# Kernel tuning notes

Measured on AMD Instinct MI355X. Metric: run time of the kernel, lower is better.

Reference implementation:

```python
import jax, jax.numpy as jnp
import numpy as np

EPS = 1e-5


def _batchnorm(x, gamma, beta):
    # training-mode batch norm over the node axis, per feature channel
    mean = jnp.mean(x, axis=0)
    var = jnp.var(x, axis=0)  # biased variance, as torch uses for normalization
    return (x - mean) * jax.lax.rsqrt(var + EPS) * gamma + beta


def _gcn_conv(h, W, b, src, dst, norm, n_nodes):
    # h: [N, Fin] -> [N, Fout]; D^{-1/2}(A+I)D^{-1/2} (h W) + b
    h = h @ W                                   # [N, Fout]
    msgs = h[src] * norm[:, None]               # [E+N, Fout] gathered, normalized
    out = jax.ops.segment_sum(msgs, dst, num_segments=n_nodes)
    return out + b


def setup_inputs() -> dict:
    key = jax.random.key(0)
    ks = jax.random.split(key, 8)
    N, F, E, H = 50000, 512, 800000, 256
    inp = {
        "x": jax.random.normal(ks[0], (N, F), jnp.float32),
        "edge_index": jax.random.randint(ks[1], (2, E), 0, N, jnp.int64),
        "gamma1": jnp.ones((F,), jnp.float32),
        "beta1": jnp.zeros((F,), jnp.float32),
        "W1": jax.random.normal(ks[2], (F, H), jnp.float32) * (1.0 / np.sqrt(F)),
        "b1": jnp.zeros((H,), jnp.float32),
        "W2": jax.random.normal(ks[3], (H, H), jnp.float32) * (1.0 / np.sqrt(H)),
        "b2": jnp.zeros((H,), jnp.float32),
        "W3": jax.random.normal(ks[4], (H, H), jnp.float32) * (1.0 / np.sqrt(H)),
        "b3": jnp.zeros((H,), jnp.float32),
        "W4": jax.random.normal(ks[5], (H, H), jnp.float32) * (1.0 / np.sqrt(H)),
        "b4": jnp.zeros((H,), jnp.float32),
        "gamma2": jnp.ones((H,), jnp.float32),
        "beta2": jnp.zeros((H,), jnp.float32),
        "Wd": jax.random.normal(ks[6], (H, 5), jnp.float32) * (1.0 / np.sqrt(H)),
        "bd": jnp.zeros((5,), jnp.float32),
    }
    return inp


def reference(x, edge_index, gamma1, beta1, W1, b1, W2, b2, W3, b3, W4, b4,
              gamma2, beta2, Wd, bd):
    N = x.shape[0]
    loops = jnp.arange(N, dtype=edge_index.dtype)
    src = jnp.concatenate([edge_index[0], loops])
    dst = jnp.concatenate([edge_index[1], loops])
    deg = jax.ops.segment_sum(jnp.ones_like(src, dtype=x.dtype), dst, num_segments=N)
    dinv = jax.lax.rsqrt(deg)                    # deg >= 1 due to self-loops
    norm = dinv[src] * dinv[dst]                 # [E+N]

    h = _batchnorm(x, gamma1, beta1)
    h = _gcn_conv(h, W1, b1, src, dst, norm, N)
    h = _gcn_conv(h, W2, b2, src, dst, norm, N)
    h = _gcn_conv(h, W3, b3, src, dst, norm, N)
    h = _gcn_conv(h, W4, b4, src, dst, norm, N)
    h = _batchnorm(h, gamma2, beta2)
    # Flatten(start_dim=1) is identity on [N, 256]
    return jax.nn.sigmoid(h @ Wd + bd)           # [N, 5]
```

## Files before the change

### kernel.cpp

```cpp
#include <hip/hip_runtime.h>
#include <math.h>

#define BN_EPS 1e-5f

typedef float floatx4 __attribute__((ext_vector_type(4)));
typedef short shortx4 __attribute__((ext_vector_type(4)));
typedef short shortx8 __attribute__((ext_vector_type(8)));
typedef __bf16 bf16x8 __attribute__((ext_vector_type(8)));

__device__ __forceinline__ unsigned short f2b(float f) {
    unsigned int u = __builtin_bit_cast(unsigned int, f);
    u += 0x7fffu + ((u >> 16) & 1u);
    return (unsigned short)(u >> 16);
}
__device__ __forceinline__ float b2f(unsigned short s) {
    unsigned int u = ((unsigned int)s) << 16;
    return __builtin_bit_cast(float, u);
}
__device__ __forceinline__ float b2f_s(short s) { return b2f((unsigned short)s); }

__global__ __launch_bounds__(256)
void k_detect(const unsigned int* __restrict__ ei, int n_check, int* __restrict__ flag) {
    __shared__ int any;
    if (threadIdx.x == 0) any = 0;
    __syncthreads();
    for (int i = threadIdx.x; i < n_check; i += 256) {
        if (ei[2 * i + 1] != 0u) any = 1;
    }
    __syncthreads();
    if (threadIdx.x == 0) *flag = any;
}

__global__ __launch_bounds__(256)
void k_convert(const void* __restrict__ ei_raw, const int* __restrict__ flag,
               int* __restrict__ src, int* __restrict__ dst, int* __restrict__ cnt, int E) {
    int e = blockIdx.x * 256 + threadIdx.x;
    if (e >= E) return;
    int s, d;
    if (*flag) {
        const int* a = (const int*)ei_raw;
        s = a[e]; d = a[E + e];
    } else {
        const long long* a = (const long long*)ei_raw;
        s = (int)a[e]; d = (int)a[E + e];
    }
    src[e] = s;
    dst[e] = d;
    atomicAdd(&cnt[d], 1);
}

__global__ __launch_bounds__(1024)
void k_scan_sum(const int* __restrict__ cnt, int* __restrict__ bsum, int N) {
    __shared__ int s[1024];
    int i = blockIdx.x * 1024 + threadIdx.x;
    s[threadIdx.x] = (i < N) ? cnt[i] : 0;
    __syncthreads();
    for (int off = 512; off > 0; off >>= 1) {
        if (threadIdx.x < off) s[threadIdx.x] += s[threadIdx.x + off];
        __syncthreads();
    }
    if (threadIdx.x == 0) bsum[blockIdx.x] = s[0];
}

__global__ __launch_bounds__(1024)
void k_scan_part(int* __restrict__ bsum, int nb) {
    __shared__ int s[1024];
    int t = threadIdx.x;
    int v = (t < nb) ? bsum[t] : 0;
    s[t] = v;
    __syncthreads();
    for (int off = 1; off < 1024; off <<= 1) {
        int tmp = (t >= off) ? s[t - off] : 0;
        __syncthreads();
        s[t] += tmp;
        __syncthreads();
    }
    if (t < nb) bsum[t] = s[t] - v;
}

__global__ __launch_bounds__(1024)
void k_scan_final(const int* __restrict__ cnt, const int* __restrict__ bsum,
                  int* __restrict__ row_ptr, int* __restrict__ cursor,
                  float* __restrict__ dinv, int N) {
    __shared__ int s[1024];
    int b = blockIdx.x, t = threadIdx.x;
    int i = b * 1024 + t;
    int v = (i < N) ? cnt[i] : 0;
    s[t] = v;
    __syncthreads();
    for (int off = 1; off < 1024; off <<= 1) {
        int tmp = (t >= off) ? s[t - off] : 0;
        __syncthreads();
        s[t] += tmp;
        __syncthreads();
    }
    if (i < N) {
        int excl = bsum[b] + s[t] - v;
        row_ptr[i] = excl;
        cursor[i]  = excl;
        dinv[i] = rsqrtf((float)(v + 1));
        if (i == N - 1) row_ptr[N] = excl + v;
    }
}

__global__ __launch_bounds__(256)
void k_fill(const int* __restrict__ src, const int* __restrict__ dst,
            int* __restrict__ cursor, const float* __restrict__ dinv,
            int2* __restrict__ csr_sw, int E) {
    int e = blockIdx.x * 256 + threadIdx.x;
    if (e >= E) return;
    int s = src[e], d = dst[e];
    int p = atomicAdd(&cursor[d], 1);
    float w = dinv[s] * dinv[d];
    csr_sw[p] = make_int2(s, __builtin_bit_cast(int, w));
}

__global__ __launch_bounds__(256)
void k_bnstats_cast(const float* __restrict__ x, unsigned short* __restrict__ xb,
                    float* __restrict__ sum8, float* __restrict__ sumsq8,
                    int NQ, int F) {
    __shared__ float ls[512], lq[512];
    int t   = threadIdx.x;
    int tid = blockIdx.x * 256 + t;
    int G   = gridDim.x * 256;
    int cq  = tid & ((F >> 2) - 1);
    const floatx4* xv = (const floatx4*)x;
    shortx4* xo = (shortx4*)xb;

    float s0 = 0.f, s1 = 0.f, s2 = 0.f, s3 = 0.f;
    float q0 = 0.f, q1 = 0.f, q2 = 0.f, q3 = 0.f;

    int G4 = G << 2;
    int Qfull = NQ - (NQ % G4);
    int i = tid;
    for (; i < Qfull; i += G4) {
        floatx4 a = __builtin_nontemporal_load(&xv[i]);
        floatx4 b = __builtin_nontemporal_load(&xv[i + G]);
        floatx4 c = __builtin_nontemporal_load(&xv[i + 2 * G]);
        floatx4 d = __builtin_nontemporal_load(&xv[i + 3 * G]);
        shortx4 o;
        o[0] = (short)f2b(a[0]); o[1] = (short)f2b(a[1]);
        o[2] = (short)f2b(a[2]); o[3] = (short)f2b(a[3]);
        xo[i] = o;
        s0 += a[0]; s1 += a[1]; s2 += a[2]; s3 += a[3];
        q0 += a[0] * a[0]; q1 += a[1] * a[1]; q2 += a[2] * a[2]; q3 += a[3] * a[3];
        o[0] = (short)f2b(b[0]); o[1] = (short)f2b(b[1]);
        o[2] = (short)f2b(b[2]); o[3] = (short)f2b(b[3]);
        xo[i + G] = o;
        s0 += b[0]; s1 += b[1]; s2 += b[2]; s3 += b[3];
        q0 += b[0] * b[0]; q1 += b[1] * b[1]; q2 += b[2] * b[2]; q3 += b[3] * b[3];
        o[0] = (short)f2b(c[0]); o[1] = (short)f2b(c[1]);
        o[2] = (short)f2b(c[2]); o[3] = (short)f2b(c[3]);
        xo[i + 2 * G] = o;
        s0 += c[0]; s1 += c[1]; s2 += c[2]; s3 += c[3];
        q0 += c[0] * c[0]; q1 += c[1] * c[1]; q2 += c[2] * c[2]; q3 += c[3] * c[3];
        o[0] = (short)f2b(d[0]); o[1] = (short)f2b(d[1]);
        o[2] = (short)f2b(d[2]); o[3] = (short)f2b(d[3]);
        xo[i + 3 * G] = o;
        s0 += d[0]; s1 += d[1]; s2 += d[2]; s3 += d[3];
        q0 += d[0] * d[0]; q1 += d[1] * d[1]; q2 += d[2] * d[2]; q3 += d[3] * d[3];
    }
    for (; i < NQ; i += G) {
        floatx4 a = __builtin_nontemporal_load(&xv[i]);
        shortx4 o;
        o[0] = (short)f2b(a[0]); o[1] = (short)f2b(a[1]);
        o[2] = (short)f2b(a[2]); o[3] = (short)f2b(a[3]);
        xo[i] = o;
        s0 += a[0]; s1 += a[1]; s2 += a[2]; s3 += a[3];
        q0 += a[0] * a[0]; q1 += a[1] * a[1]; q2 += a[2] * a[2]; q3 += a[3] * a[3];
    }

    for (int c = t; c < F; c += 256) { ls[c] = 0.f; lq[c] = 0.f; }
    __syncthreads();
    atomicAdd(&ls[cq * 4 + 0], s0); atomicAdd(&ls[cq * 4 + 1], s1);
    atomicAdd(&ls[cq * 4 + 2], s2); atomicAdd(&ls[cq * 4 + 3], s3);
    atomicAdd(&lq[cq * 4 + 0], q0); atomicAdd(&lq[cq * 4 + 1], q1);
    atomicAdd(&lq[cq * 4 + 2], q2); atomicAdd(&lq[cq * 4 + 3], q3);
    __syncthreads();
    int rep = (blockIdx.x & 7) * F;
    for (int c = t; c < F; c += 256) {
        atomicAdd(&sum8[rep + c],   ls[c]);
        atomicAdd(&sumsq8[rep + c], lq[c]);
    }
}

__global__ __launch_bounds__(256)
void k_bnstats_b(const unsigned short* __restrict__ x, float* __restrict__ sum,
                 float* __restrict__ sumsq, int NG, int H) {
    __shared__ float ls[256], lq[256];
    int t   = threadIdx.x;
    int tid = blockIdx.x * 256 + t;
    int G   = gridDim.x * 256;
    int cg  = tid & ((H >> 3) - 1);
    const shortx8* xv = (const shortx8*)x;
    float s[8], q[8];
    #pragma unroll
    for (int j = 0; j < 8; ++j) { s[j] = 0.f; q[j] = 0.f; }

    int G2 = G << 1;
    int Qfull = NG - (NG % G2);
    int i = tid;
    for (; i < Qfull; i += G2) {
        shortx8 a = __builtin_nontemporal_load(&xv[i]);
        shortx8 b = __builtin_nontemporal_load(&xv[i + G]);
        #pragma unroll
        for (int j = 0; j < 8; ++j) {
            float fa = b2f_s(a[j]);
            float fb = b2f_s(b[j]);
            s[j] += fa + fb;
            q[j] += fa * fa + fb * fb;
        }
    }
    for (; i < NG; i += G) {
        shortx8 a = __builtin_nontemporal_load(&xv[i]);
        #pragma unroll
        for (int j = 0; j < 8; ++j) {
            float fa = b2f_s(a[j]);
            s[j] += fa; q[j] += fa * fa;
        }
    }

    ls[t] = 0.f; lq[t] = 0.f;
    __syncthreads();
    #pragma unroll
    for (int j = 0; j < 8; ++j) {
        atomicAdd(&ls[cg * 8 + j], s[j]);
        atomicAdd(&lq[cg * 8 + j], q[j]);
    }
    __syncthreads();
    int rep = (blockIdx.x & 3) * H;
    atomicAdd(&sum[rep + t],   ls[t]);
    atomicAdd(&sumsq[rep + t], lq[t]);
}

__global__ __launch_bounds__(256)
void k_bnfin(const float* __restrict__ sum, const float* __restrict__ sumsq,
             const float* __restrict__ gamma, const float* __restrict__ beta,
             float* __restrict__ a, float* __restrict__ b, int N, int F, int nrep) {
    int c = blockIdx.x * 256 + threadIdx.x;
    if (c >= F) return;
    float s = 0.f, ss = 0.f;
    for (int i = 0; i < nrep; ++i) { s += sum[i * F + c]; ss += sumsq[i * F + c]; }
    float m   = s / (float)N;
    float var = ss / (float)N - m * m;
    float rs  = rsqrtf(var + BN_EPS);
    float aa  = gamma[c] * rs;
    a[c] = aa;
    b[c] = beta[c] - m * aa;
}

__global__ __launch_bounds__(256)
void k_castWT4(const float* __restrict__ W1, const float* __restrict__ W2,
               const float* __restrict__ W3, const float* __restrict__ W4,
               unsigned short* __restrict__ T1, unsigned short* __restrict__ T2,
               unsigned short* __restrict__ T3, unsigned short* __restrict__ T4,
               const float* __restrict__ bna, int F, int H) {
    int i = blockIdx.x * 256 + threadIdx.x;
    int n1 = F * H, n2 = H * H;
    if (i < n1) {
        int n = i / F, k = i % F;
        T1[i] = f2b(W1[(size_t)k * H + n] * bna[k]);
        return;
    }
    const float* W; unsigned short* T; int j;
    if (i < n1 + n2)          { W = W2; T = T2; j = i - n1; }
    else if (i < n1 + 2 * n2) { W = W3; T = T3; j = i - n1 - n2; }
    else if (i < n1 + 3 * n2) { W = W4; T = T4; j = i - n1 - 2 * n2; }
    else return;
    int n = j / H, k = j % H;
    T[j] = f2b(W[(size_t)k * H + n]);
}

__global__ __launch_bounds__(256)
void k_cvec(const float* __restrict__ W1, const float* __restrict__ bnb,
            float* __restrict__ cvec, int F, int H) {
    int j = threadIdx.x;
    int kslice = F / 8;
    int k0 = blockIdx.x * kslice;
    float s = 0.f;
    for (int k = k0; k < k0 + kslice; ++k)
        s += bnb[k] * W1[(size_t)k * H + j];
    atomicAdd(&cvec[j], s);
}

__device__ __forceinline__ void glds16(const void* g, void* l) {
    __builtin_amdgcn_global_load_lds(
        (const __attribute__((address_space(1))) unsigned int*)g,
        (__attribute__((address_space(3))) unsigned int*)l, 16, 0, 0);
}

__global__ __launch_bounds__(256)
void k_gemm_bf16(const unsigned short* __restrict__ A, const unsigned short* __restrict__ Bt,
                 unsigned short* __restrict__ C, int K, int NC) {
    __shared__ unsigned short As[128 * 32];
    __shared__ unsigned short Bs[128 * 32];
    int tid  = threadIdx.x;
    int wave = tid >> 6, lane = tid & 63;
    int row0 = blockIdx.x * 128;
    int col0 = blockIdx.y * 128;
    int wr = (wave & 1) * 64;
    int wc = (wave >> 1) * 64;

    floatx4 acc[4][4];
    #pragma unroll
    for (int i = 0; i < 4; i++)
        #pragma unroll
        for (int j = 0; j < 4; j++) acc[i][j] = (floatx4){0.f, 0.f, 0.f, 0.f};

    int cA = tid * 16;
    int cB = cA + 4096;
    const char* Ab = (const char*)A;
    const char* Bb = (const char*)Bt;
    size_t a_off0 = (size_t)(row0 + (cA >> 6)) * K * 2 + (cA & 63);
    size_t a_off1 = (size_t)(row0 + (cB >> 6)) * K * 2 + (cB & 63);
    size_t b_off0 = (size_t)(col0 + (cA >> 6)) * K * 2 + (cA & 63);
    size_t b_off1 = (size_t)(col0 + (cB >> 6)) * K * 2 + (cB & 63);

    int lm  = lane & 15;
    int lk8 = (lane >> 4) * 8;

    for (int ks = 0; ks < K; ks += 32) {
        size_t koff = (size_t)ks * 2;
        glds16(Ab + a_off0 + koff, (char*)As + cA);
        glds16(Ab + a_off1 + koff, (char*)As + cA + 4096);
        glds16(Bb + b_off0 + koff, (char*)Bs + cA);
        glds16(Bb + b_off1 + koff, (char*)Bs + cA + 4096);
        __syncthreads();

        bf16x8 af[4], bfr[4];
        #pragma unroll
        for (int i = 0; i < 4; i++) {
            shortx8 s = *(const shortx8*)&As[(wr + i * 16 + lm) * 32 + lk8];
            af[i] = __builtin_bit_cast(bf16x8, s);
        }
        #pragma unroll
        for (int j = 0; j < 4; j++) {
            shortx8 s = *(const shortx8*)&Bs[(wc + j * 16 + lm) * 32 + lk8];
            bfr[j] = __builtin_bit_cast(bf16x8, s);
        }
        #pragma unroll
        for (int i = 0; i < 4; i++)
            #pragma unroll
            for (int j = 0; j < 4; j++)
                acc[i][j] = __builtin_amdgcn_mfma_f32_16x16x32_bf16(af[i], bfr[j], acc[i][j], 0, 0, 0);
        __syncthreads();
    }

    int crow = row0 + wr + (lane >> 4) * 4;
    int ccol = col0 + wc + lm;
    #pragma unroll
    for (int i = 0; i < 4; i++)
        #pragma unroll
        for (int j = 0; j < 4; j++)
            #pragma unroll
            for (int r = 0; r < 4; r++)
                C[(size_t)(crow + i * 16 + r) * NC + ccol + j * 16] = f2b(acc[i][j][r]);
}

__global__ __launch_bounds__(256)
void k_agg(const unsigned short* __restrict__ hin, unsigned short* __restrict__ hout,
           const int* __restrict__ row_ptr, const int2* __restrict__ csr_sw,
           const float* __restrict__ dinv, const float* __restrict__ bias,
           const float* __restrict__ cvec, int N) {
    const int H = 256;
    int node = blockIdx.x * 4 + (threadIdx.x >> 6);
    if (node >= N) return;
    int lane = threadIdx.x & 63;
    int half = lane >> 5;
    int f = (lane & 31) * 8;
    float acc[8];
    float ws;
    float di = dinv[node];
    if (half == 0) {
        shortx8 hv = *(const shortx8*)&hin[(size_t)node * H + f];
        float sl = di * di;
        ws = sl;
        #pragma unroll
        for (int j = 0; j < 8; ++j) acc[j] = b2f_s(hv[j]) * sl;
    } else {
        ws = 0.f;
        #pragma unroll
        for (int j = 0; j < 8; ++j) acc[j] = 0.f;
    }
    int e0 = row_ptr[node], e1 = row_ptr[node + 1];
    int e = e0;
    int nb8 = (e1 - e0) >> 3;
    if (nb8 > 0) {
        const long long* cs = (const long long*)csr_sw;
        long long n0 = __builtin_nontemporal_load(&cs[e + 0 + half]);
        long long n1 = __builtin_nontemporal_load(&cs[e + 2 + half]);
        long long n2 = __builtin_nontemporal_load(&cs[e + 4 + half]);
        long long n3 = __builtin_nontemporal_load(&cs[e + 6 + half]);
        for (int b = 0; b < nb8; ++b) {
            long long c0 = n0, c1 = n1, c2 = n2, c3 = n3;
            int en = e + 8;
            if (b + 1 < nb8) {
                n0 = __builtin_nontemporal_load(&cs[en + 0 + half]);
                n1 = __builtin_nontemporal_load(&cs[en + 2 + half]);
                n2 = __builtin_nontemporal_load(&cs[en + 4 + half]);
                n3 = __builtin_nontemporal_load(&cs[en + 6 + half]);
            }
            int s0 = (int)c0, s1 = (int)c1, s2 = (int)c2, s3 = (int)c3;
            float w0 = __builtin_bit_cast(float, (int)(c0 >> 32));
            float w1 = __builtin_bit_cast(float, (int)(c1 >> 32));
            float w2 = __builtin_bit_cast(float, (int)(c2 >> 32));
            float w3 = __builtin_bit_cast(float, (int)(c3 >> 32));
            shortx8 r0 = *(const shortx8*)&hin[(size_t)s0 * H + f];
            shortx8 r1 = *(const shortx8*)&hin[(size_t)s1 * H + f];
            shortx8 r2 = *(const shortx8*)&hin[(size_t)s2 * H + f];
            shortx8 r3 = *(const shortx8*)&hin[(size_t)s3 * H + f];
            ws += (w0 + w1) + (w2 + w3);
            #pragma unroll
            for (int j = 0; j < 8; ++j)
                acc[j] += w0 * b2f_s(r0[j]) + w1 * b2f_s(r1[j])
                        + w2 * b2f_s(r2[j]) + w3 * b2f_s(r3[j]);
            e = en;
        }
    }
    for (; e < e1; e += 2) {
        int idx = e + half;
        bool valid = idx < e1;
        int2 pr = csr_sw[valid ? idx : e];
        float w = valid ? __builtin_bit_cast(float, pr.y) : 0.f;
        shortx8 r = *(const shortx8*)&hin[(size_t)pr.x * H + f];
        ws += w;
        #pragma unroll
        for (int j = 0; j < 8; ++j) acc[j] += w * b2f_s(r[j]);
    }
    #pragma unroll
    for (int j = 0; j < 8; ++j) acc[j] += __shfl_xor(acc[j], 32, 64);
    ws += __shfl_xor(ws, 32, 64);
    if (half == 0) {
        float4 bi0 = *(const float4*)&bias[f];
        float4 bi1 = *(const float4*)&bias[f + 4];
        if (cvec) {
            float4 c0 = *(const float4*)&cvec[f];
            float4 c1 = *(const float4*)&cvec[f + 4];
            bi0.x += ws * c0.x; bi0.y += ws * c0.y;
            bi0.z += ws * c0.z; bi0.w += ws * c0.w;
            bi1.x += ws * c1.x; bi1.y += ws * c1.y;
            bi1.z += ws * c1.z; bi1.w += ws * c1.w;
        }
        shortx8 o;
        o[0] = (short)f2b(acc[0] + bi0.x);
        o[1] = (short)f2b(acc[1] + bi0.y);
        o[2] = (short)f2b(acc[2] + bi0.z);
        o[3] = (short)f2b(acc[3] + bi0.w);
        o[4] = (short)f2b(acc[4] + bi1.x);
        o[5] = (short)f2b(acc[5] + bi1.y);
        o[6] = (short)f2b(acc[6] + bi1.z);
        o[7] = (short)f2b(acc[7] + bi1.w);
        __builtin_nontemporal_store(o, (shortx8*)&hout[(size_t)node * H + f]);
    }
}

__global__ __launch_bounds__(256)
void k_head(const unsigned short* __restrict__ h, const float* __restrict__ a,
            const float* __restrict__ b, const float* __restrict__ Wd,
            const float* __restrict__ bd, float* __restrict__ out, int N) {
    int node = blockIdx.x * 4 + (threadIdx.x >> 6);
    if (node >= N) return;
    int lane = threadIdx.x & 63;
    int f = lane * 4;
    shortx4 hv = *(const shortx4*)&h[(size_t)node * 256 + f];
    float v0 = b2f_s(hv[0]) * a[f + 0] + b[f + 0];
    float v1 = b2f_s(hv[1]) * a[f + 1] + b[f + 1];
    float v2 = b2f_s(hv[2]) * a[f + 2] + b[f + 2];
    float v3 = b2f_s(hv[3]) * a[f + 3] + b[f + 3];
    float s[5];
    #pragma unroll
    for (int j = 0; j < 5; ++j) {
        s[j] = v0 * Wd[(f + 0) * 5 + j] + v1 * Wd[(f + 1) * 5 + j] +
               v2 * Wd[(f + 2) * 5 + j] + v3 * Wd[(f + 3) * 5 + j];
    }
    #pragma unroll
    for (int off = 32; off > 0; off >>= 1) {
        #pragma unroll
        for (int j = 0; j < 5; ++j) s[j] += __shfl_down(s[j], off, 64);
    }
    if (lane == 0) {
        #pragma unroll
        for (int j = 0; j < 5; ++j) {
            float z = s[j] + bd[j];
            out[(size_t)node * 5 + j] = 1.f / (1.f + expf(-z));
        }
    }
}

extern "C" void kernel_launch(void* const* d_in, const int* in_sizes, int n_in,
                              void* d_out, int out_size, void* d_ws, size_t ws_size,
                              hipStream_t stream) {
    const float* x      = (const float*)d_in[0];
    const void*  ei_raw = d_in[1];
    const float* gamma1 = (const float*)d_in[2];
    const float* beta1  = (const float*)d_in[3];
    const float* W1 = (const float*)d_in[4];
    const float* b1 = (const float*)d_in[5];
    const float* W2 = (const float*)d_in[6];
    const float* b2 = (const float*)d_in[7];
    const float* W3 = (const float*)d_in[8];
    const float* b3 = (const float*)d_in[9];
    const float* W4 = (const float*)d_in[10];
    const float* b4 = (const float*)d_in[11];
    const float* gamma2 = (const float*)d_in[12];
    const float* beta2  = (const float*)d_in[13];
    const float* Wd = (const float*)d_in[14];
    const float* bd = (const float*)d_in[15];

    const int F = in_sizes[2];
    const int N = in_sizes[0] / F;
    const int E = in_sizes[1] / 2;
    const int H = in_sizes[5];
    const int Mpad = ((N + 127) / 128) * 128;
    const int NB   = (N + 1023) / 1024;
    float* out = (float*)d_out;

    char* p = (char*)d_ws;
    auto alloc = [&](size_t bytes) {
        void* r = (void*)p;
        p += (bytes + 255) & ~(size_t)255;
        return r;
    };
    int*   flag    = (int*)  alloc(4);
    int*   srcA    = (int*)  alloc((size_t)E * 4);
    int*   dstA    = (int*)  alloc((size_t)E * 4);
    char*  zstart  = p;
    int*   cnt     = (int*)  alloc((size_t)N * 4);
    float* colsum8 = (float*)alloc((size_t)8 * F * 4);
    float* colsq8  = (float*)alloc((size_t)8 * F * 4);
    float* colsum2 = (float*)alloc((size_t)4 * H * 4);
    float* colsq2  = (float*)alloc((size_t)4 * H * 4);
    float* cvec    = (float*)alloc((size_t)H * 4);
    size_t zbytes  = (size_t)(p - zstart);
    int*   row_ptr = (int*)  alloc(((size_t)N + 1) * 4);
    int*   cursor  = (int*)  alloc((size_t)N * 4);
    float* dinv    = (float*)alloc((size_t)N * 4);
    int2*  csr_sw  = (int2*) alloc((size_t)E * 8);
    int*   bsum    = (int*)  alloc((size_t)NB * 4);
    float* bna     = (float*)alloc((size_t)F * 4);
    float* bnb     = (float*)alloc((size_t)F * 4);
    unsigned short* W1t = (unsigned short*)alloc((size_t)F * H * 2);
    unsigned short* W2t = (unsigned short*)alloc((size_t)H * H * 2);
    unsigned short* W3t = (unsigned short*)alloc((size_t)H * H * 2);
    unsigned short* W4t = (unsigned short*)alloc((size_t)H * H * 2);
    unsigned short* xb  = (unsigned short*)alloc((size_t)Mpad * F * 2);
    unsigned short* hbA = (unsigned short*)alloc((size_t)Mpad * H * 2);
    unsigned short* hbB = (unsigned short*)alloc((size_t)Mpad * H * 2);

    hipMemsetAsync(zstart, 0, zbytes, stream);
    hipMemsetAsync(xb + (size_t)N * F, 0, (size_t)(Mpad - N) * F * 2, stream);

    int n_check = (E >= 2048) ? 2048 : E;
    k_detect<<<1, 256, 0, stream>>>((const unsigned int*)ei_raw, n_check, flag);
    k_convert<<<(E + 255) / 256, 256, 0, stream>>>(ei_raw, flag, srcA, dstA, cnt, E);
    k_scan_sum<<<NB, 1024, 0, stream>>>(cnt, bsum, N);
    k_scan_part<<<1, 1024, 0, stream>>>(bsum, NB);
    k_scan_final<<<NB, 1024, 0, stream>>>(cnt, bsum, row_ptr, cursor, dinv, N);
    k_fill<<<(E + 255) / 256, 256, 0, stream>>>(srcA, dstA, cursor, dinv, csr_sw, E);

    int NQ = N * (F >> 2);
    k_bnstats_cast<<<2048, 256, 0, stream>>>(x, xb, colsum8, colsq8, NQ, F);
    k_bnfin<<<(F + 255) / 256, 256, 0, stream>>>(colsum8, colsq8, gamma1, beta1, bna, bnb, N, F, 8);

    int tot = F * H + 3 * H * H;
    k_castWT4<<<(tot + 255) / 256, 256, 0, stream>>>(W1, W2, W3, W4, W1t, W2t, W3t, W4t, bna, F, H);
    k_cvec<<<8, 256, 0, stream>>>(W1, bnb, cvec, F, H);

    dim3 gg(Mpad / 128, H / 128);
    int aggb = (N + 3) / 4;
    k_gemm_bf16<<<gg, 256, 0, stream>>>(xb, W1t, hbA, F, H);
    k_agg<<<aggb, 256, 0, stream>>>(hbA, hbB, row_ptr, csr_sw, dinv, b1, cvec, N);
    k_gemm_bf16<<<gg, 256, 0, stream>>>(hbB, W2t, hbA, H, H);
    k_agg<<<aggb, 256, 0, stream>>>(hbA, hbB, row_ptr, csr_sw, dinv, b2, nullptr, N);
    k_gemm_bf16<<<gg, 256, 0, stream>>>(hbB, W3t, hbA, H, H);
    k_agg<<<aggb, 256, 0, stream>>>(hbA, hbB, row_ptr, csr_sw, dinv, b3, nullptr, N);
    k_gemm_bf16<<<gg, 256, 0, stream>>>(hbB, W4t, hbA, H, H);
    k_agg<<<aggb, 256, 0, stream>>>(hbA, hbB, row_ptr, csr_sw, dinv, b4, nullptr, N);

    int NG = N * (H >> 3);
    k_bnstats_b<<<1024, 256, 0, stream>>>(hbB, colsum2, colsq2, NG, H);
    k_bnfin<<<(H + 255) / 256, 256, 0, stream>>>(colsum2, colsq2, gamma2, beta2, bna, bnb, N, H, 4);
    k_head<<<(N + 3) / 4, 256, 0, stream>>>(hbB, bna, bnb, Wd, bd, out, N);
}
```

Measured before the change: 704.5 us.

## Store hidden features in 32-column feature-sliced layout for cache-local aggregation

```diff
diff --git a/kernel.cpp b/kernel.cpp
--- a/kernel.cpp
+++ b/kernel.cpp
@@ -186,20 +186,23 @@
 
 __global__ __launch_bounds__(256)
 void k_bnstats_b(const unsigned short* __restrict__ x, float* __restrict__ sum,
-                 float* __restrict__ sumsq, int NG, int H) {
+                 float* __restrict__ sumsq, int N, int Mpad, int H) {
     __shared__ float ls[256], lq[256];
-    int t   = threadIdx.x;
-    int tid = blockIdx.x * 256 + t;
-    int G   = gridDim.x * 256;
-    int cg  = tid & ((H >> 3) - 1);
-    const shortx8* xv = (const shortx8*)x;
+    int t     = threadIdx.x;
+    int slice = blockIdx.x & 7;
+    int bs    = blockIdx.x >> 3;
+    int tid_s = bs * 256 + t;
+    int G     = (gridDim.x >> 3) * 256;
+    int NG    = N * 4;
+    const shortx8* xv = (const shortx8*)x + (size_t)slice * Mpad * 4;
+    int fq = tid_s & 3;
     float s[8], q[8];
     #pragma unroll
     for (int j = 0; j < 8; ++j) { s[j] = 0.f; q[j] = 0.f; }
 
     int G2 = G << 1;
     int Qfull = NG - (NG % G2);
-    int i = tid;
+    int i = tid_s;
     for (; i < Qfull; i += G2) {
         shortx8 a = __builtin_nontemporal_load(&xv[i]);
         shortx8 b = __builtin_nontemporal_load(&xv[i + G]);
@@ -222,15 +225,18 @@
 
     ls[t] = 0.f; lq[t] = 0.f;
     __syncthreads();
+    int fg = slice * 4 + fq;
     #pragma unroll
     for (int j = 0; j < 8; ++j) {
-        atomicAdd(&ls[cg * 8 + j], s[j]);
-        atomicAdd(&lq[cg * 8 + j], q[j]);
-    }
-    __syncthreads();
-    int rep = (blockIdx.x & 3) * H;
-    atomicAdd(&sum[rep + t],   ls[t]);
-    atomicAdd(&sumsq[rep + t], lq[t]);
+        atomicAdd(&ls[fg * 8 + j], s[j]);
+        atomicAdd(&lq[fg * 8 + j], q[j]);
+    }
+    __syncthreads();
+    int rep = (bs & 3) * H;
+    if ((t >> 5) == slice) {
+        atomicAdd(&sum[rep + t],   ls[t]);
+        atomicAdd(&sumsq[rep + t], lq[t]);
+    }
 }
 
 __global__ __launch_bounds__(256)
@@ -291,7 +297,8 @@
 
 __global__ __launch_bounds__(256)
 void k_gemm_bf16(const unsigned short* __restrict__ A, const unsigned short* __restrict__ Bt,
-                 unsigned short* __restrict__ C, int K, int NC) {
+                 unsigned short* __restrict__ C, int K, int NC,
+                 size_t arow, size_t aks, size_t Mslice) {
     __shared__ unsigned short As[128 * 32];
     __shared__ unsigned short Bs[128 * 32];
     int tid  = threadIdx.x;
@@ -311,18 +318,19 @@
     int cB = cA + 4096;
     const char* Ab = (const char*)A;
     const char* Bb = (const char*)Bt;
-    size_t a_off0 = (size_t)(row0 + (cA >> 6)) * K * 2 + (cA & 63);
-    size_t a_off1 = (size_t)(row0 + (cB >> 6)) * K * 2 + (cB & 63);
+    size_t a_off0 = (size_t)(row0 + (cA >> 6)) * arow + (cA & 63);
+    size_t a_off1 = (size_t)(row0 + (cB >> 6)) * arow + (cA & 63);
     size_t b_off0 = (size_t)(col0 + (cA >> 6)) * K * 2 + (cA & 63);
-    size_t b_off1 = (size_t)(col0 + (cB >> 6)) * K * 2 + (cB & 63);
+    size_t b_off1 = (size_t)(col0 + (cB >> 6)) * K * 2 + (cA & 63);
 
     int lm  = lane & 15;
     int lk8 = (lane >> 4) * 8;
 
     for (int ks = 0; ks < K; ks += 32) {
-        size_t koff = (size_t)ks * 2;
-        glds16(Ab + a_off0 + koff, (char*)As + cA);
-        glds16(Ab + a_off1 + koff, (char*)As + cA + 4096);
+        size_t abase = (size_t)ks * aks;
+        size_t koff  = (size_t)ks * 2;
+        glds16(Ab + a_off0 + abase, (char*)As + cA);
+        glds16(Ab + a_off1 + abase, (char*)As + cA + 4096);
         glds16(Bb + b_off0 + koff, (char*)Bs + cA);
         glds16(Bb + b_off1 + koff, (char*)Bs + cA + 4096);
         __syncthreads();
@@ -347,95 +355,82 @@
     }
 
     int crow = row0 + wr + (lane >> 4) * 4;
-    int ccol = col0 + wc + lm;
-    #pragma unroll
-    for (int i = 0; i < 4; i++)
-        #pragma unroll
-        for (int j = 0; j < 4; j++)
+    int ccol0 = col0 + wc + lm;
+    #pragma unroll
+    for (int j = 0; j < 4; j++) {
+        int c = ccol0 + j * 16;
+        size_t cb = (size_t)(c >> 5) * Mslice + (c & 31);
+        #pragma unroll
+        for (int i = 0; i < 4; i++)
             #pragma unroll
             for (int r = 0; r < 4; r++)
-                C[(size_t)(crow + i * 16 + r) * NC + ccol + j * 16] = f2b(acc[i][j][r]);
+                C[cb + (size_t)(crow + i * 16 + r) * 32] = f2b(acc[i][j][r]);
+    }
 }
 
 __global__ __launch_bounds__(256)
 void k_agg(const unsigned short* __restrict__ hin, unsigned short* __restrict__ hout,
            const int* __restrict__ row_ptr, const int2* __restrict__ csr_sw,
            const float* __restrict__ dinv, const float* __restrict__ bias,
-           const float* __restrict__ cvec, int N) {
-    const int H = 256;
-    int node = blockIdx.x * 4 + (threadIdx.x >> 6);
+           const float* __restrict__ cvec, int N, int Mpad) {
+    int slice = blockIdx.x & 7;
+    int nb    = blockIdx.x >> 3;
+    int tid   = threadIdx.x;
+    int node  = nb * 16 + (tid >> 4);
     if (node >= N) return;
-    int lane = threadIdx.x & 63;
-    int half = lane >> 5;
-    int f = (lane & 31) * 8;
+    int eg = (tid >> 2) & 3;
+    int fl = tid & 3;
+    size_t sbase = (size_t)slice * Mpad * 32;
+    const unsigned short* hs = hin + sbase;
+
     float acc[8];
-    float ws;
+    float ws = 0.f;
+    #pragma unroll
+    for (int j = 0; j < 8; ++j) acc[j] = 0.f;
     float di = dinv[node];
-    if (half == 0) {
-        shortx8 hv = *(const shortx8*)&hin[(size_t)node * H + f];
+    if (eg == 0) {
+        shortx8 hv = *(const shortx8*)&hs[(size_t)node * 32 + fl * 8];
         float sl = di * di;
         ws = sl;
         #pragma unroll
         for (int j = 0; j < 8; ++j) acc[j] = b2f_s(hv[j]) * sl;
-    } else {
-        ws = 0.f;
-        #pragma unroll
-        for (int j = 0; j < 8; ++j) acc[j] = 0.f;
-    }
+    }
+
     int e0 = row_ptr[node], e1 = row_ptr[node + 1];
-    int e = e0;
-    int nb8 = (e1 - e0) >> 3;
-    if (nb8 > 0) {
-        const long long* cs = (const long long*)csr_sw;
-        long long n0 = __builtin_nontemporal_load(&cs[e + 0 + half]);
-        long long n1 = __builtin_nontemporal_load(&cs[e + 2 + half]);
-        long long n2 = __builtin_nontemporal_load(&cs[e + 4 + half]);
-        long long n3 = __builtin_nontemporal_load(&cs[e + 6 + half]);
-        for (int b = 0; b < nb8; ++b) {
-            long long c0 = n0, c1 = n1, c2 = n2, c3 = n3;
-            int en = e + 8;
-            if (b + 1 < nb8) {
-                n0 = __builtin_nontemporal_load(&cs[en + 0 + half]);
-                n1 = __builtin_nontemporal_load(&cs[en + 2 + half]);
-                n2 = __builtin_nontemporal_load(&cs[en + 4 + half]);
-                n3 = __builtin_nontemporal_load(&cs[en + 6 + half]);
-            }
-            int s0 = (int)c0, s1 = (int)c1, s2 = (int)c2, s3 = (int)c3;
-            float w0 = __builtin_bit_cast(float, (int)(c0 >> 32));
-            float w1 = __builtin_bit_cast(float, (int)(c1 >> 32));
-            float w2 = __builtin_bit_cast(float, (int)(c2 >> 32));
-            float w3 = __builtin_bit_cast(float, (int)(c3 >> 32));
-            shortx8 r0 = *(const shortx8*)&hin[(size_t)s0 * H + f];
-            shortx8 r1 = *(const shortx8*)&hin[(size_t)s1 * H + f];
-            shortx8 r2 = *(const shortx8*)&hin[(size_t)s2 * H + f];
-            shortx8 r3 = *(const shortx8*)&hin[(size_t)s3 * H + f];
-            ws += (w0 + w1) + (w2 + w3);
-            #pragma unroll
-            for (int j = 0; j < 8; ++j)
-                acc[j] += w0 * b2f_s(r0[j]) + w1 * b2f_s(r1[j])
-                        + w2 * b2f_s(r2[j]) + w3 * b2f_s(r3[j]);
-            e = en;
-        }
-    }
-    for (; e < e1; e += 2) {
-        int idx = e + half;
-        bool valid = idx < e1;
-        int2 pr = csr_sw[valid ? idx : e];
-        float w = valid ? __builtin_bit_cast(float, pr.y) : 0.f;
-        shortx8 r = *(const shortx8*)&hin[(size_t)pr.x * H + f];
-        ws += w;
-        #pragma unroll
-        for (int j = 0; j < 8; ++j) acc[j] += w * b2f_s(r[j]);
-    }
-    #pragma unroll
-    for (int j = 0; j < 8; ++j) acc[j] += __shfl_xor(acc[j], 32, 64);
-    ws += __shfl_xor(ws, 32, 64);
-    if (half == 0) {
-        float4 bi0 = *(const float4*)&bias[f];
-        float4 bi1 = *(const float4*)&bias[f + 4];
+    const long long* cs = (const long long*)csr_sw;
+    for (int e = e0; e < e1; e += 8) {
+        int ia = e + eg;
+        int ib = e + 4 + eg;
+        bool va = ia < e1;
+        bool vb = ib < e1;
+        long long pa = __builtin_nontemporal_load(&cs[va ? ia : e0]);
+        long long pb = __builtin_nontemporal_load(&cs[vb ? ib : e0]);
+        int sa = (int)pa, sb = (int)pb;
+        float wa = va ? __builtin_bit_cast(float, (int)(pa >> 32)) : 0.f;
+        float wb = vb ? __builtin_bit_cast(float, (int)(pb >> 32)) : 0.f;
+        shortx8 ra = *(const shortx8*)&hs[(size_t)sa * 32 + fl * 8];
+        shortx8 rb = *(const shortx8*)&hs[(size_t)sb * 32 + fl * 8];
+        ws += wa + wb;
+        #pragma unroll
+        for (int j = 0; j < 8; ++j)
+            acc[j] += wa * b2f_s(ra[j]) + wb * b2f_s(rb[j]);
+    }
+
+    #pragma unroll
+    for (int j = 0; j < 8; ++j) {
+        acc[j] += __shfl_xor(acc[j], 4, 64);
+        acc[j] += __shfl_xor(acc[j], 8, 64);
+    }
+    ws += __shfl_xor(ws, 4, 64);
+    ws += __shfl_xor(ws, 8, 64);
+
+    if (eg == 0) {
+        int g = slice * 32 + fl * 8;
+        float4 bi0 = *(const float4*)&bias[g];
+        float4 bi1 = *(const float4*)&bias[g + 4];
         if (cvec) {
-            float4 c0 = *(const float4*)&cvec[f];
-            float4 c1 = *(const float4*)&cvec[f + 4];
+            float4 c0 = *(const float4*)&cvec[g];
+            float4 c1 = *(const float4*)&cvec[g + 4];
             bi0.x += ws * c0.x; bi0.y += ws * c0.y;
             bi0.z += ws * c0.z; bi0.w += ws * c0.w;
             bi1.x += ws * c1.x; bi1.y += ws * c1.y;
@@ -450,19 +445,21 @@
         o[5] = (short)f2b(acc[5] + bi1.y);
         o[6] = (short)f2b(acc[6] + bi1.z);
         o[7] = (short)f2b(acc[7] + bi1.w);
-        __builtin_nontemporal_store(o, (shortx8*)&hout[(size_t)node * H + f]);
+        __builtin_nontemporal_store(o, (shortx8*)&hout[sbase + (size_t)node * 32 + fl * 8]);
     }
 }
 
 __global__ __launch_bounds__(256)
 void k_head(const unsigned short* __restrict__ h, const float* __restrict__ a,
             const float* __restrict__ b, const float* __restrict__ Wd,
-            const float* __restrict__ bd, float* __restrict__ out, int N) {
+            const float* __restrict__ bd, float* __restrict__ out, int N, int Mpad) {
     int node = blockIdx.x * 4 + (threadIdx.x >> 6);
     if (node >= N) return;
     int lane = threadIdx.x & 63;
     int f = lane * 4;
-    shortx4 hv = *(const shortx4*)&h[(size_t)node * 256 + f];
+    int slice = lane >> 3;
+    int off = (lane & 7) * 4;
+    shortx4 hv = *(const shortx4*)&h[(size_t)slice * Mpad * 32 + (size_t)node * 32 + off];
     float v0 = b2f_s(hv[0]) * a[f + 0] + b[f + 0];
     float v1 = b2f_s(hv[1]) * a[f + 1] + b[f + 1];
     float v2 = b2f_s(hv[2]) * a[f + 2] + b[f + 2];
@@ -474,9 +471,9 @@
                v2 * Wd[(f + 2) * 5 + j] + v3 * Wd[(f + 3) * 5 + j];
     }
     #pragma unroll
-    for (int off = 32; off > 0; off >>= 1) {
-        #pragma unroll
-        for (int j = 0; j < 5; ++j) s[j] += __shfl_down(s[j], off, 64);
+    for (int off2 = 32; off2 > 0; off2 >>= 1) {
+        #pragma unroll
+        for (int j = 0; j < 5; ++j) s[j] += __shfl_down(s[j], off2, 64);
     }
     if (lane == 0) {
         #pragma unroll
@@ -513,6 +510,7 @@
     const int H = in_sizes[5];
     const int Mpad = ((N + 127) / 128) * 128;
     const int NB   = (N + 1023) / 1024;
+    const size_t Mslice = (size_t)Mpad * 32;
     float* out = (float*)d_out;
 
     char* p = (char*)d_ws;
@@ -567,18 +565,20 @@
     k_cvec<<<8, 256, 0, stream>>>(W1, bnb, cvec, F, H);
 
     dim3 gg(Mpad / 128, H / 128);
-    int aggb = (N + 3) / 4;
-    k_gemm_bf16<<<gg, 256, 0, stream>>>(xb, W1t, hbA, F, H);
-    k_agg<<<aggb, 256, 0, stream>>>(hbA, hbB, row_ptr, csr_sw, dinv, b1, cvec, N);
-    k_gemm_bf16<<<gg, 256, 0, stream>>>(hbB, W2t, hbA, H, H);
-    k_agg<<<aggb, 256, 0, stream>>>(hbA, hbB, row_ptr, csr_sw, dinv, b2, nullptr, N);
-    k_gemm_bf16<<<gg, 256, 0, stream>>>(hbB, W3t, hbA, H, H);
-    k_agg<<<aggb, 256, 0, stream>>>(hbA, hbB, row_ptr, csr_sw, dinv, b3, nullptr, N);
-    k_gemm_bf16<<<gg, 256, 0, stream>>>(hbB, W4t, hbA, H, H);
-    k_agg<<<aggb, 256, 0, stream>>>(hbA, hbB, row_ptr, csr_sw, dinv, b4, nullptr, N);
-
-    int NG = N * (H >> 3);
-    k_bnstats_b<<<1024, 256, 0, stream>>>(hbB, colsum2, colsq2, NG, H);
+    int aggb = ((N + 15) / 16) * 8;
+    size_t arow_rm = (size_t)F * 2;
+    size_t arow_sm = 64;
+    size_t aks_sm  = (size_t)Mpad * 2;
+    k_gemm_bf16<<<gg, 256, 0, stream>>>(xb, W1t, hbA, F, H, arow_rm, 2, Mslice);
+    k_agg<<<aggb, 256, 0, stream>>>(hbA, hbB, row_ptr, csr_sw, dinv, b1, cvec, N, Mpad);
+    k_gemm_bf16<<<gg, 256, 0, stream>>>(hbB, W2t, hbA, H, H, arow_sm, aks_sm, Mslice);
+    k_agg<<<aggb, 256, 0, stream>>>(hbA, hbB, row_ptr, csr_sw, dinv, b2, nullptr, N, Mpad);
+    k_gemm_bf16<<<gg, 256, 0, stream>>>(hbB, W3t, hbA, H, H, arow_sm, aks_sm, Mslice);
+    k_agg<<<aggb, 256, 0, stream>>>(hbA, hbB, row_ptr, csr_sw, dinv, b3, nullptr, N, Mpad);
+    k_gemm_bf16<<<gg, 256, 0, stream>>>(hbB, W4t, hbA, H, H, arow_sm, aks_sm, Mslice);
+    k_agg<<<aggb, 256, 0, stream>>>(hbA, hbB, row_ptr, csr_sw, dinv, b4, nullptr, N, Mpad);
+
+    k_bnstats_b<<<1024, 256, 0, stream>>>(hbB, colsum2, colsq2, N, Mpad, H);
     k_bnfin<<<(H + 255) / 256, 256, 0, stream>>>(colsum2, colsq2, gamma2, beta2, bna, bnb, N, H, 4);
-    k_head<<<(N + 3) / 4, 256, 0, stream>>>(hbB, bna, bnb, Wd, bd, out, N);
-}
+    k_head<<<(N + 3) / 4, 256, 0, stream>>>(hbB, bna, bnb, Wd, bd, out, N, Mpad);
+}
```

Result: slower. 836.4 us (+18.7%).
